# Optimization experiments

Measured on AMD Instinct MI355X. Metric: run time of the kernel, lower is better.

## Reference

```python
import jax, jax.numpy as jnp
import numpy as np

N_SOC = 100_000   # nodes in social_neighbour_g (== embedding rows)
N_I2U = 50_000    # nodes in item2user_g
E_SOC = 1_600_000
E_I2U = 800_000
F = 128           # embedding_size (num_heads = 1)


def gatv2(src, dst, num_nodes, feat, Ws, bs, Wd, bd, attn):
    """DGL GATv2Conv, num_heads=1, share_weights=False, activation=leaky_relu."""
    el = feat @ Ws + bs                     # [N, F] fc_src
    er = feat @ Wd + bd                     # [N, F] fc_dst
    e = jax.nn.leaky_relu(el[src] + er[dst], 0.2)   # [E, F]
    s = e @ attn                            # [E] attention logits
    # edge softmax grouped by destination node
    m = jax.ops.segment_max(s, dst, num_segments=num_nodes)
    ex = jnp.exp(s - m[dst])
    den = jax.ops.segment_sum(ex, dst, num_segments=num_nodes)
    alpha = ex / den[dst]                   # [E]
    out = jax.ops.segment_sum(el[src] * alpha[:, None], dst, num_segments=num_nodes)
    return jax.nn.leaky_relu(out, 0.01)     # module-level activation (default slope)


def setup_inputs() -> dict:
    key = jax.random.key(0)
    ks = jax.random.split(key, 16)
    sc = 1.0 / np.sqrt(F)
    inp = {
        "embedding": jax.random.normal(ks[0], (N_SOC, F), jnp.float32),
        "i2u_src": jax.random.randint(ks[1], (E_I2U,), 0, N_I2U, jnp.int32),
        "i2u_dst": jax.random.randint(ks[2], (E_I2U,), 0, N_I2U, jnp.int32),
        "i2u_nid": jnp.arange(N_I2U, dtype=jnp.int32),  # unique global IDs of subgraph nodes
        "soc_src": jax.random.randint(ks[3], (E_SOC,), 0, N_SOC, jnp.int32),
        "soc_dst": jax.random.randint(ks[4], (E_SOC,), 0, N_SOC, jnp.int32),
        "Wsrc1": jax.random.normal(ks[5], (F, F), jnp.float32) * sc,
        "bsrc1": jnp.zeros((F,), jnp.float32),
        "Wdst1": jax.random.normal(ks[6], (F, F), jnp.float32) * sc,
        "bdst1": jnp.zeros((F,), jnp.float32),
        "attn1": jax.random.normal(ks[7], (F,), jnp.float32) * sc,
        "Wsrc2": jax.random.normal(ks[8], (F, F), jnp.float32) * sc,
        "bsrc2": jnp.zeros((F,), jnp.float32),
        "Wdst2": jax.random.normal(ks[9], (F, F), jnp.float32) * sc,
        "bdst2": jnp.zeros((F,), jnp.float32),
        "attn2": jax.random.normal(ks[10], (F,), jnp.float32) * sc,
    }
    return inp


def reference(embedding, i2u_src, i2u_dst, i2u_nid, soc_src, soc_dst,
              Wsrc1, bsrc1, Wdst1, bdst1, attn1,
              Wsrc2, bsrc2, Wdst2, bdst2, attn2):
    # social_used_embedding = embedding[item2user_g.ndata['_ID']]
    used = embedding[i2u_nid]                                   # [N_i2u, F]
    h1 = gatv2(i2u_src, i2u_dst, i2u_nid.shape[0], used,
               Wsrc1, bsrc1, Wdst1, bdst1, attn1)               # [N_i2u, F]
    # social_embedding = embedding[social_g.nodes()]  (nodes() == arange(N_soc))
    soc = embedding
    # used_user_id = where(sum(h1, dim=1) != 0); scatter those rows via _ID
    mask = jnp.sum(h1, axis=1) != 0                              # [N_i2u]
    upd = jnp.where(mask[:, None], h1, soc[i2u_nid])
    soc = soc.at[i2u_nid].set(upd)
    out = gatv2(soc_src, soc_dst, soc.shape[0], soc,
                Wsrc2, bsrc2, Wdst2, bdst2, attn2)               # [N_soc, F]
    return out
```

## Files before the change

### kernel.cpp

```cpp
#include <hip/hip_runtime.h>
#include <hip/hip_fp16.h>
#include <math.h>

#define F 128
#define BSHIFT 9
#define BSIZE  512
#define BMAX   200
#define CHUNK  4096
#define PKSTR  12288

#define APAD 8
#define ASTR (F + APAD)

typedef _Float16 half8_t __attribute__((ext_vector_type(8)));
typedef _Float16 half4_t __attribute__((ext_vector_type(4)));
typedef float f32x4 __attribute__((ext_vector_type(4)));

#define PK_ADD(d, a, b) asm("v_pk_add_f16 %0, %1, %2" : "=v"(d) : "v"(a), "v"(b))
#define PK_MUL(d, a, b) asm("v_pk_mul_f16 %0, %1, %2" : "=v"(d) : "v"(a), "v"(b))
#define PK_MAX(d, a, b) asm("v_pk_max_f16 %0, %1, %2" : "=v"(d) : "v"(a), "v"(b))
#define FMA_MIX_LO(acc, h2u, f) \
    asm("v_fma_mix_f32 %0, %1, %2, %0 op_sel_hi:[1,0,0]" : "+v"(acc) : "v"(h2u), "v"(f))
#define FMA_MIX_HI(acc, h2u, f) \
    asm("v_fma_mix_f32 %0, %1, %2, %0 op_sel:[1,0,0] op_sel_hi:[1,0,0]" : "+v"(acc) : "v"(h2u), "v"(f))

__device__ __forceinline__ float row_sum16(float x) {
    int y;
    y = __builtin_amdgcn_update_dpp(0, __float_as_int(x), 0x121, 0xf, 0xf, true);
    x += __int_as_float(y);
    y = __builtin_amdgcn_update_dpp(0, __float_as_int(x), 0x122, 0xf, 0xf, true);
    x += __int_as_float(y);
    y = __builtin_amdgcn_update_dpp(0, __float_as_int(x), 0x124, 0xf, 0xf, true);
    x += __int_as_float(y);
    y = __builtin_amdgcn_update_dpp(0, __float_as_int(x), 0x128, 0xf, 0xf, true);
    x += __int_as_float(y);
    return x;
}

__global__ __launch_bounds__(256) void k_scatter(
        const int* __restrict__ src1, const int* __restrict__ dst1, int E1,
        int* __restrict__ bcur1, unsigned* __restrict__ pk1, int C1,
        const int* __restrict__ src2, const int* __restrict__ dst2, int E2,
        int* __restrict__ bcur2, unsigned* __restrict__ pk2, int C2,
        const int* __restrict__ nid, int Nn, int* __restrict__ inv, int CI,
        const float* __restrict__ Ws1, const float* __restrict__ Wd1,
        const float* __restrict__ bs1, const float* __restrict__ bd1,
        __half* __restrict__ wt1, float* __restrict__ bp1,
        const float* __restrict__ Ws2, const float* __restrict__ Wd2,
        const float* __restrict__ bs2, const float* __restrict__ bd2,
        __half* __restrict__ wt2, float* __restrict__ bp2) {
    int b = blockIdx.x, t = threadIdx.x;
    __shared__ int hist[BMAX];
    __shared__ int cur[BMAX];
    if (b < C1 + C2) {
        const int* src; const int* dst; int E; int* bcur; unsigned* pk; int c;
        if (b < C1) { src = src1; dst = dst1; E = E1; bcur = bcur1; pk = pk1; c = b; }
        else        { src = src2; dst = dst2; E = E2; bcur = bcur2; pk = pk2; c = b - C1; }
        for (int i = t; i < BMAX; i += 256) hist[i] = 0;
        __syncthreads();
        int e0 = c * CHUNK;
        int dc[CHUNK / 256], sc[CHUNK / 256];
#pragma unroll
        for (int i = 0; i < CHUNK / 256; i++) {
            int e = e0 + t + i * 256;
            if (e < E) {
                int d = dst[e];
                dc[i] = d; sc[i] = src[e];
                atomicAdd(&hist[d >> BSHIFT], 1);
            } else {
                dc[i] = -1;
            }
        }
        __syncthreads();
        for (int i = t; i < BMAX; i += 256) {
            int n = hist[i];
            if (n) cur[i] = atomicAdd(&bcur[i], n);
        }
        __syncthreads();
#pragma unroll
        for (int i = 0; i < CHUNK / 256; i++) {
            int d = dc[i];
            if (d >= 0) {
                int bb = d >> BSHIFT;
                int pos = atomicAdd(&cur[bb], 1);
                if (pos < PKSTR)
                    pk[(size_t)bb * PKSTR + pos] =
                        ((unsigned)(d & (BSIZE - 1)) << 17) | (unsigned)sc[i];
            }
        }
    } else if (b < C1 + C2 + CI) {
        int i0 = (b - C1 - C2) * CHUNK + t;
#pragma unroll
        for (int k = 0; k < CHUNK / 256; k++) {
            int j = i0 + k * 256;
            if (j < Nn) inv[nid[j]] = j;
        }
    } else {
        int wb = b - (C1 + C2 + CI);
        int layer = wb >> 3, bl = wb & 7;
        const float* Ws = layer ? Ws2 : Ws1;
        const float* Wd = layer ? Wd2 : Wd1;
        __half* wt = layer ? wt2 : wt1;
#pragma unroll
        for (int i = 0; i < 16; i++) {
            int e = bl * 4096 + i * 256 + t;
            int n = e >> 7, k = e & 127;
            float v = (n < 128) ? Ws[k * 128 + n] : Wd[k * 128 + (n - 128)];
            wt[(size_t)n * 128 + k] = __float2half(v);
        }
        if (bl == 0) {
            const float* bs = layer ? bs2 : bs1;
            const float* bd = layer ? bd2 : bd1;
            float* bp = layer ? bp2 : bp1;
            bp[t] = (t < 128) ? bs[t] : bd[t - 128];
        }
    }
}

__global__ void k_scan(
        const int* __restrict__ cnt1, int B1, int* __restrict__ bbase1,
        int* __restrict__ rp1, int N1,
        const int* __restrict__ cnt2, int B2, int* __restrict__ bbase2,
        int* __restrict__ rp2, int N2) {
    __shared__ int s[BMAX + 1];
    const int* cnt; int B; int* bbase; int* rp; int N;
    if (blockIdx.x == 0) { cnt = cnt1; B = B1; bbase = bbase1; rp = rp1; N = N1; }
    else                 { cnt = cnt2; B = B2; bbase = bbase2; rp = rp2; N = N2; }
    int t = threadIdx.x;
    for (int i = t; i < B; i += 256) {
        int v = cnt[i];
        s[i] = v < PKSTR ? v : PKSTR;
    }
    __syncthreads();
    if (t == 0) {
        int acc = 0;
        for (int i = 0; i < B; i++) { int v = s[i]; s[i] = acc; acc += v; }
        s[B] = acc;
    }
    __syncthreads();
    for (int i = t; i <= B; i += 256) bbase[i] = s[i];
    if (t == 0) rp[N] = s[B];
}

__global__ __launch_bounds__(256) void k_finesort(
        const unsigned* __restrict__ pk1, const int* __restrict__ bbase1, int B1, int N1,
        int* __restrict__ rp1, int* __restrict__ out1,
        const unsigned* __restrict__ pk2, const int* __restrict__ bbase2, int N2,
        int* __restrict__ rp2, int* __restrict__ out2) {
    int blk = blockIdx.x, t = threadIdx.x;
    const unsigned* pk; const int* bbase; int N; int* rp; int* out; int b;
    if (blk < B1) { pk = pk1; bbase = bbase1; N = N1; rp = rp1; out = out1; b = blk; }
    else          { pk = pk2; bbase = bbase2; N = N2; rp = rp2; out = out2; b = blk - B1; }
    __shared__ int cnt[BSIZE];
    __shared__ int cur[BSIZE];
    __shared__ int tps[256];
    int node0 = b << BSHIFT;
    int ebeg = bbase[b], eend = bbase[b + 1];
    int ne = eend - ebeg;
    const unsigned* pkb = pk + (size_t)b * PKSTR;
    cnt[t] = 0; cnt[t + 256] = 0;
    __syncthreads();
    for (int i = t; i < ne; i += 256) atomicAdd(&cnt[pkb[i] >> 17], 1);
    __syncthreads();
    int s0 = cnt[2 * t], s1 = cnt[2 * t + 1];
    int tp = s0 + s1;
    tps[t] = tp;
    __syncthreads();
    for (int off = 1; off < 256; off <<= 1) {
        int x = (t >= off) ? tps[t - off] : 0;
        __syncthreads();
        tps[t] += x;
        __syncthreads();
    }
    int excl = tps[t] - tp;
    int c0 = ebeg + excl, c1 = c0 + s0;
    cur[2 * t] = c0; cur[2 * t + 1] = c1;
    int n0 = node0 + 2 * t, n1 = n0 + 1;
    if (n0 < N) rp[n0] = c0;
    if (n1 < N) rp[n1] = c1;
    __syncthreads();
    for (int i = t; i < ne; i += 256) {
        unsigned v = pkb[i];
        int dl = v >> 17;
        int pos = atomicAdd(&cur[dl], 1);
        out[pos] = (int)(v & 0x1FFFFu);
    }
}

__device__ __forceinline__ void gemm_mfma_body(int blk,
        const float* __restrict__ emb, const int* __restrict__ nid,
        const float* __restrict__ h1, const int* __restrict__ inv, const int* __restrict__ flag,
        int Nrows,
        const __half* __restrict__ wt, const float* __restrict__ bp,
        __half* __restrict__ el, __half* __restrict__ er) {
    __shared__ _Float16 As[64 * ASTR];
    __shared__ const float* rps[64];
    int t = threadIdx.x;
    int row0 = blk * 64;

    if (t < 64) {
        int grow = row0 + t;
        const float* rowp = nullptr;
        if (grow < Nrows) {
            if (inv) {
                int j = inv[grow];
                rowp = (j >= 0 && flag[j]) ? h1 + (size_t)j * F : emb + (size_t)grow * F;
            } else {
                int asrc = nid ? nid[grow] : grow;
                rowp = emb + (size_t)asrc * F;
            }
        }
        rps[t] = rowp;
    }
    __syncthreads();

#pragma unroll
    for (int i = 0; i < 8; i++) {
        int e = i * 256 + t;
        int r = e >> 5;
        int c = (e & 31) * 4;
        const float* rowp = rps[r];
        float4 v = make_float4(0.f, 0.f, 0.f, 0.f);
        if (rowp) v = *(const float4*)(rowp + c);
        half4_t hv = { (_Float16)v.x, (_Float16)v.y, (_Float16)v.z, (_Float16)v.w };
        *(half4_t*)(As + r * ASTR + c) = hv;
    }
    __syncthreads();

    int lane = t & 63, wave = t >> 6;
    int li = lane & 15, quad = lane >> 4;

    f32x4 acc[4][4];
#pragma unroll
    for (int a = 0; a < 4; a++)
#pragma unroll
        for (int b = 0; b < 4; b++) acc[a][b] = (f32x4){0.f, 0.f, 0.f, 0.f};

    const _Float16* wtp = (const _Float16*)wt;
#pragma unroll
    for (int ks = 0; ks < 4; ks++) {
        half8_t af[4], bf[4];
#pragma unroll
        for (int nt = 0; nt < 4; nt++)
            af[nt] = *(const half8_t*)(As + (nt * 16 + li) * ASTR + ks * 32 + quad * 8);
#pragma unroll
        for (int ft = 0; ft < 4; ft++) {
            int n = wave * 64 + ft * 16 + li;
            bf[ft] = *(const half8_t*)(wtp + (size_t)n * F + ks * 32 + quad * 8);
        }
#pragma unroll
        for (int ft = 0; ft < 4; ft++)
#pragma unroll
            for (int nt = 0; nt < 4; nt++)
                acc[ft][nt] = __builtin_amdgcn_mfma_f32_16x16x32_f16(
                    bf[ft], af[nt], acc[ft][nt], 0, 0, 0);
    }

    __half* dst = (wave < 2) ? el : er;
    int fb = (wave & 1) * 64 + quad * 4;
    f32x4 bv4[4];
#pragma unroll
    for (int ft = 0; ft < 4; ft++)
        bv4[ft] = *(const f32x4*)(bp + wave * 64 + ft * 16 + quad * 4);
#pragma unroll
    for (int nt = 0; nt < 4; nt++) {
        int node = row0 + nt * 16 + li;
        if (node < Nrows) {
#pragma unroll
            for (int ft = 0; ft < 4; ft++) {
                half4_t h4 = { (_Float16)(acc[ft][nt][0] + bv4[ft][0]),
                               (_Float16)(acc[ft][nt][1] + bv4[ft][1]),
                               (_Float16)(acc[ft][nt][2] + bv4[ft][2]),
                               (_Float16)(acc[ft][nt][3] + bv4[ft][3]) };
                *(half4_t*)(dst + (size_t)node * F + fb + ft * 16) = h4;
            }
        }
    }
}

__global__ __launch_bounds__(256, 4) void gemm1_k(
        const float* __restrict__ emb, const int* __restrict__ nid, int Nrows,
        const __half* __restrict__ wt, const float* __restrict__ bp,
        __half* __restrict__ el, __half* __restrict__ er) {
    gemm_mfma_body(blockIdx.x, emb, nid, nullptr, nullptr, nullptr, Nrows, wt, bp, el, er);
}

__global__ __launch_bounds__(256, 4) void gemm2_k(
        const float* __restrict__ emb, const float* __restrict__ h1,
        const int* __restrict__ inv, const int* __restrict__ flag, int Nrows,
        const __half* __restrict__ wt, const float* __restrict__ bp,
        __half* __restrict__ el, __half* __restrict__ er) {
    gemm_mfma_body(blockIdx.x, emb, nullptr, h1, inv, flag, Nrows, wt, bp, el, er);
}

__device__ __forceinline__ void agg_core(
        const int* __restrict__ rowptr, const int* __restrict__ srcs,
        const __half* __restrict__ el, const __half* __restrict__ er,
        const float* __restrict__ attn, int node, int g, int li,
        float* o, int& beg, int& end) {
    uint4 ru = *(const uint4*)(er + (size_t)node * F + li * 8);
    float av[8];
    *(float4*)(av + 0) = *(const float4*)(attn + li * 8 + 0);
    *(float4*)(av + 4) = *(const float4*)(attn + li * 8 + 4);
#pragma unroll
    for (int j = 0; j < 8; j++) av[j] *= 1.44269504f;

    beg = rowptr[node]; end = rowptr[node + 1];
    float l = 0.f;
    float acc[8];
#pragma unroll
    for (int j = 0; j < 8; j++) acc[j] = 0.f;

    const unsigned C02 = 0x32663266u;

    auto dot_edge = [&](const uint4& V) -> float {
        float p = 0.f;
        unsigned x, y;
        PK_ADD(x, V.x, ru.x); PK_MUL(y, x, C02); PK_MAX(x, x, y);
        FMA_MIX_LO(p, x, av[0]); FMA_MIX_HI(p, x, av[1]);
        PK_ADD(x, V.y, ru.y); PK_MUL(y, x, C02); PK_MAX(x, x, y);
        FMA_MIX_LO(p, x, av[2]); FMA_MIX_HI(p, x, av[3]);
        PK_ADD(x, V.z, ru.z); PK_MUL(y, x, C02); PK_MAX(x, x, y);
        FMA_MIX_LO(p, x, av[4]); FMA_MIX_HI(p, x, av[5]);
        PK_ADD(x, V.w, ru.w); PK_MUL(y, x, C02); PK_MAX(x, x, y);
        FMA_MIX_LO(p, x, av[6]); FMA_MIX_HI(p, x, av[7]);
        return p;
    };
    auto acc_edge = [&](const uint4& V, float ex) {
        FMA_MIX_LO(acc[0], V.x, ex); FMA_MIX_HI(acc[1], V.x, ex);
        FMA_MIX_LO(acc[2], V.y, ex); FMA_MIX_HI(acc[3], V.y, ex);
        FMA_MIX_LO(acc[4], V.z, ex); FMA_MIX_HI(acc[5], V.z, ex);
        FMA_MIX_LO(acc[6], V.w, ex); FMA_MIX_HI(acc[7], V.w, ex);
    };

    const __half* ep = el + li * 8;
    for (int cb = beg; cb < end; cb += 16) {
        int a0 = cb + g * 4;
        bool v0 = a0 < end, v1 = a0 + 1 < end, v2 = a0 + 2 < end, v3 = a0 + 3 < end;
        int s0 = srcs[v0 ? a0     : beg];
        int s1 = srcs[v1 ? a0 + 1 : beg];
        int s2 = srcs[v2 ? a0 + 2 : beg];
        int s3 = srcs[v3 ? a0 + 3 : beg];
        uint4 A = *(const uint4*)(ep + (size_t)s0 * F);
        uint4 B = *(const uint4*)(ep + (size_t)s1 * F);
        uint4 Cv = *(const uint4*)(ep + (size_t)s2 * F);
        uint4 D = *(const uint4*)(ep + (size_t)s3 * F);

        float p0 = dot_edge(A), p1 = dot_edge(B), p2 = dot_edge(Cv), p3 = dot_edge(D);
        p0 = row_sum16(p0); p1 = row_sum16(p1);
        p2 = row_sum16(p2); p3 = row_sum16(p3);
        float x0 = v0 ? __builtin_amdgcn_exp2f(p0) : 0.f;
        float x1 = v1 ? __builtin_amdgcn_exp2f(p1) : 0.f;
        float x2 = v2 ? __builtin_amdgcn_exp2f(p2) : 0.f;
        float x3 = v3 ? __builtin_amdgcn_exp2f(p3) : 0.f;
        l += (x0 + x1) + (x2 + x3);
        acc_edge(A, x0); acc_edge(B, x1); acc_edge(Cv, x2); acc_edge(D, x3);
    }

#pragma unroll
    for (int off = 16; off < 64; off <<= 1) {
        l += __shfl_xor(l, off, 64);
#pragma unroll
        for (int j = 0; j < 8; j++) acc[j] += __shfl_xor(acc[j], off, 64);
    }

    if (end > beg) {
        float inv = 1.f / l;
#pragma unroll
        for (int j = 0; j < 8; j++) {
            float v = acc[j] * inv;
            o[j] = fmaxf(v, 0.01f * v);
        }
    } else {
#pragma unroll
        for (int j = 0; j < 8; j++) o[j] = 0.f;
    }
}

__global__ __launch_bounds__(256) void agg1_k(
        const int* __restrict__ rowptr, const int* __restrict__ srcs,
        const __half* __restrict__ el, const __half* __restrict__ er,
        const float* __restrict__ attn, int N,
        float* __restrict__ h1, int* __restrict__ flag) {
    int node = blockIdx.x * 4 + (threadIdx.x >> 6);
    if (node >= N) return;
    int lane = threadIdx.x & 63;
    int g = lane >> 4, li = lane & 15;
    float o[8]; int beg, end;
    agg_core(rowptr, srcs, el, er, attn, node, g, li, o, beg, end);

    float tot = 0.f;
#pragma unroll
    for (int j = 0; j < 8; j++) tot += o[j];
    tot = row_sum16(tot);
    if (g == 0) {
        *(float4*)(h1 + (size_t)node * F + li * 8 + 0) = *(float4*)(o + 0);
        *(float4*)(h1 + (size_t)node * F + li * 8 + 4) = *(float4*)(o + 4);
        if (li == 0) flag[node] = (tot != 0.f) ? 1 : 0;
    }
}

__global__ __launch_bounds__(256) void agg2_k(
        const int* __restrict__ rowptr, const int* __restrict__ srcs,
        const __half* __restrict__ el, const __half* __restrict__ er,
        const float* __restrict__ attn, int N, float* __restrict__ out) {
    int node = blockIdx.x * 4 + (threadIdx.x >> 6);
    if (node >= N) return;
    int lane = threadIdx.x & 63;
    int g = lane >> 4, li = lane & 15;
    float o[8]; int beg, end;
    agg_core(rowptr, srcs, el, er, attn, node, g, li, o, beg, end);
    if (g == 0) {
        *(float4*)(out + (size_t)node * F + li * 8 + 0) = *(float4*)(o + 0);
        *(float4*)(out + (size_t)node * F + li * 8 + 4) = *(float4*)(o + 4);
    }
}

static inline int cdiv(int a, int b) { return (a + b - 1) / b; }

extern "C" void kernel_launch(void* const* d_in, const int* in_sizes, int n_in,
                              void* d_out, int out_size, void* d_ws, size_t ws_size,
                              hipStream_t stream) {
    const float* emb   = (const float*)d_in[0];
    const int* i2u_src = (const int*)d_in[1];
    const int* i2u_dst = (const int*)d_in[2];
    const int* i2u_nid = (const int*)d_in[3];
    const int* soc_src = (const int*)d_in[4];
    const int* soc_dst = (const int*)d_in[5];
    const float* Ws1 = (const float*)d_in[6];
    const float* bs1 = (const float*)d_in[7];
    const float* Wd1 = (const float*)d_in[8];
    const float* bd1 = (const float*)d_in[9];
    const float* at1 = (const float*)d_in[10];
    const float* Ws2 = (const float*)d_in[11];
    const float* bs2 = (const float*)d_in[12];
    const float* Wd2 = (const float*)d_in[13];
    const float* bd2 = (const float*)d_in[14];
    const float* at2 = (const float*)d_in[15];

    const int N_soc = in_sizes[0] / F;
    const int E_i2u = in_sizes[1];
    const int N_i2u = in_sizes[3];
    const int E_soc = in_sizes[4];

    const int B1 = cdiv(N_i2u, BSIZE);
    const int B2 = cdiv(N_soc, BSIZE);
    const int C1 = cdiv(E_i2u, CHUNK);
    const int C2 = cdiv(E_soc, CHUNK);
    const int CI = cdiv(N_i2u, CHUNK);

    char* p = (char*)d_ws;
    auto carve = [&](size_t bytes) -> char* {
        char* r = p; p += (bytes + 255) & ~(size_t)255; return r;
    };
    __half* el1  = (__half*)carve((size_t)N_i2u * F * 2);
    __half* er1  = (__half*)carve((size_t)N_i2u * F * 2);
    __half* el2  = (__half*)carve((size_t)N_soc * F * 2);
    __half* er2  = (__half*)carve((size_t)N_soc * F * 2);
    float* h1buf = (float*)carve((size_t)N_i2u * F * 4);
    int* flag    = (int*)carve((size_t)N_i2u * 4);
    int* inv     = (int*)carve((size_t)N_soc * 4);

    unsigned* pk1 = (unsigned*)carve((size_t)B1 * PKSTR * 4);
    unsigned* pk2 = (unsigned*)carve((size_t)B2 * PKSTR * 4);
    int* srcs1   = (int*)carve((size_t)E_i2u * 4);
    int* srcs2   = (int*)carve((size_t)E_soc * 4);
    int* rowptr1 = (int*)carve((size_t)(N_i2u + 1) * 4);
    int* rowptr2 = (int*)carve((size_t)(N_soc + 1) * 4);

    int* bcur    = (int*)carve((size_t)(B1 + B2) * 4);
    int* bcur1 = bcur, *bcur2 = bcur + B1;
    int* bbase1  = (int*)carve((size_t)(B1 + 1) * 4);
    int* bbase2  = (int*)carve((size_t)(B2 + 1) * 4);

    __half* wt1  = (__half*)carve((size_t)256 * 128 * 2);
    __half* wt2  = (__half*)carve((size_t)256 * 128 * 2);
    float* bp1   = (float*)carve(256 * 4);
    float* bp2   = (float*)carve(256 * 4);

    (void)hipMemsetAsync(bcur, 0, (size_t)(B1 + B2) * 4, stream);
    (void)hipMemsetAsync(inv, 0xFF, (size_t)N_soc * 4, stream);

    k_scatter<<<C1 + C2 + CI + 16, 256, 0, stream>>>(
        i2u_src, i2u_dst, E_i2u, bcur1, pk1, C1,
        soc_src, soc_dst, E_soc, bcur2, pk2, C2,
        i2u_nid, N_i2u, inv, CI,
        Ws1, Wd1, bs1, bd1, wt1, bp1,
        Ws2, Wd2, bs2, bd2, wt2, bp2);

    k_scan<<<2, 256, 0, stream>>>(
        bcur1, B1, bbase1, rowptr1, N_i2u,
        bcur2, B2, bbase2, rowptr2, N_soc);

    k_finesort<<<B1 + B2, 256, 0, stream>>>(
        pk1, bbase1, B1, N_i2u, rowptr1, srcs1,
        pk2, bbase2, N_soc, rowptr2, srcs2);

    gemm1_k<<<cdiv(N_i2u, 64), 256, 0, stream>>>(emb, i2u_nid, N_i2u, wt1, bp1, el1, er1);
    agg1_k<<<cdiv(N_i2u, 4), 256, 0, stream>>>(rowptr1, srcs1, el1, er1, at1, N_i2u, h1buf, flag);

    gemm2_k<<<cdiv(N_soc, 64), 256, 0, stream>>>(emb, h1buf, inv, flag, N_soc, wt2, bp2, el2, er2);
    agg2_k<<<cdiv(N_soc, 4), 256, 0, stream>>>(rowptr2, srcs2, el2, er2, at2, N_soc, (float*)d_out);
}
```

Before: 356.7 us.

## Use half-wavefront per node in aggregation with prefetched source indices

The aggregation kernels now give each destination node 32 lanes (two groups of 16) instead of a full 64-lane wavefront. That doubles nodes per block, cuts idle lanes on low-degree nodes (average degree about 16), and reduces the cross-group reduction to a single shuffle. The edge loop software-prefetches the next batch of source indices with nontemporal loads, to overlap index fetch with the gather. The log2(e) scaling of the attention vector is precomputed once in the setup kernel rather than per thread. In exchange each node gets less parallelism per step, so high-degree nodes take more loop iterations.

```diff
diff --git a/kernel.cpp b/kernel.cpp
--- a/kernel.cpp
+++ b/kernel.cpp
@@ -45,10 +45,12 @@
         const int* __restrict__ nid, int Nn, int* __restrict__ inv, int CI,
         const float* __restrict__ Ws1, const float* __restrict__ Wd1,
         const float* __restrict__ bs1, const float* __restrict__ bd1,
-        __half* __restrict__ wt1, float* __restrict__ bp1,
+        const float* __restrict__ at1,
+        __half* __restrict__ wt1, float* __restrict__ bp1, float* __restrict__ ap1,
         const float* __restrict__ Ws2, const float* __restrict__ Wd2,
         const float* __restrict__ bs2, const float* __restrict__ bd2,
-        __half* __restrict__ wt2, float* __restrict__ bp2) {
+        const float* __restrict__ at2,
+        __half* __restrict__ wt2, float* __restrict__ bp2, float* __restrict__ ap2) {
     int b = blockIdx.x, t = threadIdx.x;
     __shared__ int hist[BMAX];
     __shared__ int cur[BMAX];
@@ -111,8 +113,11 @@
         if (bl == 0) {
             const float* bs = layer ? bs2 : bs1;
             const float* bd = layer ? bd2 : bd1;
+            const float* at = layer ? at2 : at1;
             float* bp = layer ? bp2 : bp1;
+            float* ap = layer ? ap2 : ap1;
             bp[t] = (t < 128) ? bs[t] : bd[t - 128];
+            if (t < 128) ap[t] = at[t] * 1.44269504f;
         }
     }
 }
@@ -296,14 +301,12 @@
 __device__ __forceinline__ void agg_core(
         const int* __restrict__ rowptr, const int* __restrict__ srcs,
         const __half* __restrict__ el, const __half* __restrict__ er,
-        const float* __restrict__ attn, int node, int g, int li,
+        const float* __restrict__ ap, int node, int g, int li,
         float* o, int& beg, int& end) {
     uint4 ru = *(const uint4*)(er + (size_t)node * F + li * 8);
     float av[8];
-    *(float4*)(av + 0) = *(const float4*)(attn + li * 8 + 0);
-    *(float4*)(av + 4) = *(const float4*)(attn + li * 8 + 4);
-#pragma unroll
-    for (int j = 0; j < 8; j++) av[j] *= 1.44269504f;
+    *(float4*)(av + 0) = *(const float4*)(ap + li * 8 + 0);
+    *(float4*)(av + 4) = *(const float4*)(ap + li * 8 + 4);
 
     beg = rowptr[node]; end = rowptr[node + 1];
     float l = 0.f;
@@ -334,35 +337,45 @@
     };
 
     const __half* ep = el + li * 8;
-    for (int cb = beg; cb < end; cb += 16) {
-        int a0 = cb + g * 4;
-        bool v0 = a0 < end, v1 = a0 + 1 < end, v2 = a0 + 2 < end, v3 = a0 + 3 < end;
-        int s0 = srcs[v0 ? a0     : beg];
-        int s1 = srcs[v1 ? a0 + 1 : beg];
-        int s2 = srcs[v2 ? a0 + 2 : beg];
-        int s3 = srcs[v3 ? a0 + 3 : beg];
-        uint4 A = *(const uint4*)(ep + (size_t)s0 * F);
-        uint4 B = *(const uint4*)(ep + (size_t)s1 * F);
-        uint4 Cv = *(const uint4*)(ep + (size_t)s2 * F);
-        uint4 D = *(const uint4*)(ep + (size_t)s3 * F);
-
-        float p0 = dot_edge(A), p1 = dot_edge(B), p2 = dot_edge(Cv), p3 = dot_edge(D);
-        p0 = row_sum16(p0); p1 = row_sum16(p1);
-        p2 = row_sum16(p2); p3 = row_sum16(p3);
-        float x0 = v0 ? __builtin_amdgcn_exp2f(p0) : 0.f;
-        float x1 = v1 ? __builtin_amdgcn_exp2f(p1) : 0.f;
-        float x2 = v2 ? __builtin_amdgcn_exp2f(p2) : 0.f;
-        float x3 = v3 ? __builtin_amdgcn_exp2f(p3) : 0.f;
-        l += (x0 + x1) + (x2 + x3);
-        acc_edge(A, x0); acc_edge(B, x1); acc_edge(Cv, x2); acc_edge(D, x3);
-    }
-
-#pragma unroll
-    for (int off = 16; off < 64; off <<= 1) {
-        l += __shfl_xor(l, off, 64);
-#pragma unroll
-        for (int j = 0; j < 8; j++) acc[j] += __shfl_xor(acc[j], off, 64);
-    }
+    if (beg < end) {
+        int e1 = end - 1;
+        int a0 = beg + g * 4;
+        int s0 = __builtin_nontemporal_load(srcs + (a0     < e1 ? a0     : e1));
+        int s1 = __builtin_nontemporal_load(srcs + (a0 + 1 < e1 ? a0 + 1 : e1));
+        int s2 = __builtin_nontemporal_load(srcs + (a0 + 2 < e1 ? a0 + 2 : e1));
+        int s3 = __builtin_nontemporal_load(srcs + (a0 + 3 < e1 ? a0 + 3 : e1));
+        for (int cb = beg; cb < end; cb += 8) {
+            int c0 = cb + g * 4;
+            bool v0 = c0 < end, v1 = c0 + 1 < end, v2 = c0 + 2 < end, v3 = c0 + 3 < end;
+            int t0 = s0, t1 = s1, t2 = s2, t3 = s3;
+            int nb = cb + 8;
+            if (nb < end) {
+                int b0 = nb + g * 4;
+                s0 = __builtin_nontemporal_load(srcs + (b0     < e1 ? b0     : e1));
+                s1 = __builtin_nontemporal_load(srcs + (b0 + 1 < e1 ? b0 + 1 : e1));
+                s2 = __builtin_nontemporal_load(srcs + (b0 + 2 < e1 ? b0 + 2 : e1));
+                s3 = __builtin_nontemporal_load(srcs + (b0 + 3 < e1 ? b0 + 3 : e1));
+            }
+            uint4 A  = *(const uint4*)(ep + (size_t)t0 * F);
+            uint4 B  = *(const uint4*)(ep + (size_t)t1 * F);
+            uint4 Cv = *(const uint4*)(ep + (size_t)t2 * F);
+            uint4 D  = *(const uint4*)(ep + (size_t)t3 * F);
+
+            float p0 = dot_edge(A), p1 = dot_edge(B), p2 = dot_edge(Cv), p3 = dot_edge(D);
+            p0 = row_sum16(p0); p1 = row_sum16(p1);
+            p2 = row_sum16(p2); p3 = row_sum16(p3);
+            float x0 = v0 ? __builtin_amdgcn_exp2f(p0) : 0.f;
+            float x1 = v1 ? __builtin_amdgcn_exp2f(p1) : 0.f;
+            float x2 = v2 ? __builtin_amdgcn_exp2f(p2) : 0.f;
+            float x3 = v3 ? __builtin_amdgcn_exp2f(p3) : 0.f;
+            l += (x0 + x1) + (x2 + x3);
+            acc_edge(A, x0); acc_edge(B, x1); acc_edge(Cv, x2); acc_edge(D, x3);
+        }
+    }
+
+    l += __shfl_xor(l, 16, 64);
+#pragma unroll
+    for (int j = 0; j < 8; j++) acc[j] += __shfl_xor(acc[j], 16, 64);
 
     if (end > beg) {
         float inv = 1.f / l;
@@ -380,14 +393,14 @@
 __global__ __launch_bounds__(256) void agg1_k(
         const int* __restrict__ rowptr, const int* __restrict__ srcs,
         const __half* __restrict__ el, const __half* __restrict__ er,
-        const float* __restrict__ attn, int N,
+        const float* __restrict__ ap, int N,
         float* __restrict__ h1, int* __restrict__ flag) {
-    int node = blockIdx.x * 4 + (threadIdx.x >> 6);
+    int node = blockIdx.x * 8 + (threadIdx.x >> 5);
     if (node >= N) return;
-    int lane = threadIdx.x & 63;
-    int g = lane >> 4, li = lane & 15;
+    int t = threadIdx.x;
+    int g = (t >> 4) & 1, li = t & 15;
     float o[8]; int beg, end;
-    agg_core(rowptr, srcs, el, er, attn, node, g, li, o, beg, end);
+    agg_core(rowptr, srcs, el, er, ap, node, g, li, o, beg, end);
 
     float tot = 0.f;
 #pragma unroll
@@ -403,13 +416,13 @@
 __global__ __launch_bounds__(256) void agg2_k(
         const int* __restrict__ rowptr, const int* __restrict__ srcs,
         const __half* __restrict__ el, const __half* __restrict__ er,
-        const float* __restrict__ attn, int N, float* __restrict__ out) {
-    int node = blockIdx.x * 4 + (threadIdx.x >> 6);
+        const float* __restrict__ ap, int N, float* __restrict__ out) {
+    int node = blockIdx.x * 8 + (threadIdx.x >> 5);
     if (node >= N) return;
-    int lane = threadIdx.x & 63;
-    int g = lane >> 4, li = lane & 15;
+    int t = threadIdx.x;
+    int g = (t >> 4) & 1, li = t & 15;
     float o[8]; int beg, end;
-    agg_core(rowptr, srcs, el, er, attn, node, g, li, o, beg, end);
+    agg_core(rowptr, srcs, el, er, ap, node, g, li, o, beg, end);
     if (g == 0) {
         *(float4*)(out + (size_t)node * F + li * 8 + 0) = *(float4*)(o + 0);
         *(float4*)(out + (size_t)node * F + li * 8 + 4) = *(float4*)(o + 4);
@@ -477,6 +490,8 @@
     __half* wt2  = (__half*)carve((size_t)256 * 128 * 2);
     float* bp1   = (float*)carve(256 * 4);
     float* bp2   = (float*)carve(256 * 4);
+    float* ap1   = (float*)carve(128 * 4);
+    float* ap2   = (float*)carve(128 * 4);
 
     (void)hipMemsetAsync(bcur, 0, (size_t)(B1 + B2) * 4, stream);
     (void)hipMemsetAsync(inv, 0xFF, (size_t)N_soc * 4, stream);
@@ -485,8 +500,8 @@
         i2u_src, i2u_dst, E_i2u, bcur1, pk1, C1,
         soc_src, soc_dst, E_soc, bcur2, pk2, C2,
         i2u_nid, N_i2u, inv, CI,
-        Ws1, Wd1, bs1, bd1, wt1, bp1,
-        Ws2, Wd2, bs2, bd2, wt2, bp2);
+        Ws1, Wd1, bs1, bd1, at1, wt1, bp1, ap1,
+        Ws2, Wd2, bs2, bd2, at2, wt2, bp2, ap2);
 
     k_scan<<<2, 256, 0, stream>>>(
         bcur1, B1, bbase1, rowptr1, N_i2u,
@@ -497,8 +512,8 @@
         pk2, bbase2, N_soc, rowptr2, srcs2);
 
     gemm1_k<<<cdiv(N_i2u, 64), 256, 0, stream>>>(emb, i2u_nid, N_i2u, wt1, bp1, el1, er1);
-    agg1_k<<<cdiv(N_i2u, 4), 256, 0, stream>>>(rowptr1, srcs1, el1, er1, at1, N_i2u, h1buf, flag);
+    agg1_k<<<cdiv(N_i2u, 8), 256, 0, stream>>>(rowptr1, srcs1, el1, er1, ap1, N_i2u, h1buf, flag);
 
     gemm2_k<<<cdiv(N_soc, 64), 256, 0, stream>>>(emb, h1buf, inv, flag, N_soc, wt2, bp2, el2, er2);
-    agg2_k<<<cdiv(N_soc, 4), 256, 0, stream>>>(rowptr2, srcs2, el2, er2, at2, N_soc, (float*)d_out);
-}
+    agg2_k<<<cdiv(N_soc, 8), 256, 0, stream>>>(rowptr2, srcs2, el2, er2, ap2, N_soc, (float*)d_out);
+}
```

After: 354.1 us. No clear change (-0.7%).
